# Kernel optimization log

Measured on AMD Instinct MI355X. Metric: run time of the kernel, lower is better.

Reference implementation:

```python
import jax, jax.numpy as jnp
import numpy as np

B, D_IN, D_OUT, N_SUBNET, G = 16384, 512, 512, 8, 2


def setup_inputs() -> dict:
    key = jax.random.key(0)
    k_x, k_g, k_w = jax.random.split(key, 3)
    x = jax.random.normal(k_x, (B, D_IN), dtype=jnp.float32)
    groups = jax.random.randint(k_g, (B, G), 0, N_SUBNET, dtype=jnp.int32)
    # per-expert Dense params (the 'subnets')
    W = jax.random.normal(k_w, (N_SUBNET, D_IN, D_OUT), dtype=jnp.float32) * (1.0 / np.sqrt(D_IN))
    b = jnp.zeros((N_SUBNET, D_OUT), dtype=jnp.float32)
    return {"x": x, "groups": groups, "W": W, "b": b}


def reference(x, groups, W, b):
    """SubnetGate: one-hot gated dispatch to per-group subnets + combine.

    Faithful math: gates = one_hot(groups[:, group_col], n_subnet);
    out = sum_e gates[:, e] * subnet_e(x). Since gates are one-hot the
    combine selects exactly one expert output per row (gate weight 1.0).
    """
    group_col = 0
    n_subnet = W.shape[0]
    idx_group = groups[:, group_col]                     # [B]
    gates = jax.nn.one_hot(idx_group, n_subnet, dtype=x.dtype)  # [B, E]
    # run every expert on the full batch (dense reference for the
    # gather-compute-scatter kernel), then gate-combine
    expert_out = jnp.einsum("bi,eio->beo", x, W) + b[None, :, :]  # [B, E, O]
    out = jnp.einsum("be,beo->bo", gates, expert_out)             # [B, O]
    return out
```

## Files before the change

### kernel.cpp

```cpp
#include <hip/hip_runtime.h>
#include <hip/hip_bf16.h>


#define NROWS   16384
#define KDIM    512
#define NDIM    512
#define NEXP    8
#define TILE_ELEMS 8192
#define ATILE_ELEMS 4096
#define MAX_DESC 264
#define WS_NDESC_OFF   64
#define WS_DESC_OFF    128
#define WS_ROWLIST_OFF 4096
#define WS_WT_OFF      (4096 + NEXP * NROWS * 4)
#define WS_XG_OFF      (WS_WT_OFF + NEXP * KDIM * NDIM * 2)
#define WS_NEED        ((size_t)WS_XG_OFF + (size_t)MAX_DESC * 8 * ATILE_ELEMS * 2)

typedef __bf16        bf16x8 __attribute__((ext_vector_type(8)));
typedef float         f32x4  __attribute__((ext_vector_type(4)));
typedef unsigned int  u32x4  __attribute__((ext_vector_type(4)));

__device__ __forceinline__ unsigned int f2bf_u(float f) {
    unsigned int u = __builtin_bit_cast(unsigned int, f);
    return (u + 0x7FFFu + ((u >> 16) & 1u)) >> 16;
}
__device__ __forceinline__ unsigned int pack2(float a, float b) {
    return f2bf_u(a) | (f2bf_u(b) << 16);
}
__device__ __forceinline__ u32x4 pack8(f32x4 a, f32x4 b) {
    u32x4 p;
    p.x = pack2(a.x, a.y); p.y = pack2(a.z, a.w);
    p.z = pack2(b.x, b.y); p.w = pack2(b.z, b.w);
    return p;
}
__device__ __forceinline__ void gl_lds16(const void* g, void* l) {
    __builtin_amdgcn_global_load_lds(
        (const __attribute__((address_space(1))) unsigned int*)g,
        (__attribute__((address_space(3))) unsigned int*)l, 16, 0, 0);
}

__global__ void zero_kernel(int* __restrict__ gcnt) {
    if (threadIdx.x < NEXP) gcnt[threadIdx.x] = 0;
}

__global__ void prep_kernel(const float* __restrict__ W,
                            const int* __restrict__ groups,
                            int* __restrict__ gcnt,
                            int* __restrict__ rowlist,
                            unsigned short* __restrict__ Wtile) {
    __shared__ __align__(16) unsigned short tl[TILE_ELEMS];
    __shared__ int lcnt[NEXP];
    __shared__ int lbase[NEXP];
    const int bid = blockIdx.x;
    const int tid = threadIdx.x;

    if (bid < 256) {
        const int e  = bid >> 5;
        const int nt = (bid >> 3) & 3;
        const int kt = bid & 7;
        const float* Wb = W + (size_t)e * (KDIM * NDIM);
        #pragma unroll
        for (int i = 0; i < 4; ++i) {
            int f = i * 256 + tid;
            int n = f & 127;
            int g = f >> 7;
            int col = nt * 128 + n;
            unsigned int p[4];
            #pragma unroll
            for (int jj = 0; jj < 4; ++jj) {
                int k0 = kt * 64 + g * 8 + jj * 2;
                p[jj] = pack2(Wb[(size_t)k0 * NDIM + col],
                              Wb[(size_t)(k0 + 1) * NDIM + col]);
            }
            *(u32x4*)&tl[n * 64 + (g ^ (n & 7)) * 8] = *(const u32x4*)p;
        }
        __syncthreads();
        unsigned short* dst = Wtile + (size_t)bid * TILE_ELEMS;
        #pragma unroll
        for (int i = 0; i < 4; ++i) {
            int off = (i * 256 + tid) * 8;
            *(u32x4*)&dst[off] = *(const u32x4*)&tl[off];
        }
    } else {
        const int base = (bid - 256) * 256;
        if (tid < NEXP) lcnt[tid] = 0;
        __syncthreads();
        int r = base + tid;
        int e = groups[r * 2];
        int pos = atomicAdd(&lcnt[e], 1);
        __syncthreads();
        if (tid < NEXP) lbase[tid] = atomicAdd(&gcnt[tid], lcnt[tid]);
        __syncthreads();
        rowlist[e * NROWS + lbase[e] + pos] = r;
    }
}

__global__ void plan_kernel(const int* __restrict__ counts,
                            int* __restrict__ ndesc,
                            int* __restrict__ desc) {
    if (threadIdx.x == 0) {
        int M = 0;
        for (int e = 0; e < NEXP; ++e) {
            int nmt = (counts[e] + 63) >> 6;
            for (int mt = 0; mt < nmt && M < MAX_DESC; ++mt)
                desc[M++] = (e << 16) | mt;
        }
        ndesc[0] = M;
    }
}

__global__ __launch_bounds__(256, 4)
void gather_kernel(const float* __restrict__ x,
                   const int* __restrict__ counts,
                   const int* __restrict__ rowlist,
                   const int* __restrict__ ndesc,
                   const int* __restrict__ desc,
                   unsigned short* __restrict__ xg) {
    const int bid = blockIdx.x;
    const int d  = bid >> 3;
    const int kt = bid & 7;
    if (d >= ndesc[0]) return;
    const int de = desc[d];
    const int e  = de >> 16;
    const int mt = de & 0xffff;
    const int cnt = counts[e];
    int m_valid = cnt - mt * 64;
    if (m_valid > 64) m_valid = 64;
    const int* rl = rowlist + e * NROWS + mt * 64;

    const int t = threadIdx.x;
    const int m = t >> 2;
    const int c = t & 3;

    u32x4 lo = {0u,0u,0u,0u}, hi = {0u,0u,0u,0u};
    if (m < m_valid) {
        const float* s = x + (size_t)rl[m] * KDIM + kt * 64 + c * 16;
        f32x4 v0 = *(const f32x4*)(s);
        f32x4 v1 = *(const f32x4*)(s + 4);
        f32x4 v2 = *(const f32x4*)(s + 8);
        f32x4 v3 = *(const f32x4*)(s + 12);
        lo = pack8(v0, v1);
        hi = pack8(v2, v3);
    }
    const int p = m & 7;
    unsigned short* tile = xg + ((size_t)d * 8 + kt) * ATILE_ELEMS;
    int base = (m * 8 + ((2 * c) ^ (p & 6))) * 8;
    if (p & 1) {
        *(u32x4*)&tile[base]     = hi;
        *(u32x4*)&tile[base + 8] = lo;
    } else {
        *(u32x4*)&tile[base]     = lo;
        *(u32x4*)&tile[base + 8] = hi;
    }
}

__global__ __launch_bounds__(256, 4)
void gemm_tiled(const unsigned short* __restrict__ xg,
                const int* __restrict__ counts,
                const int* __restrict__ rowlist,
                const unsigned short* __restrict__ Wtile,
                const float* __restrict__ bias,
                float* __restrict__ out,
                const int* __restrict__ ndesc,
                const int* __restrict__ desc) {
    __shared__ __align__(16) unsigned short Asm[ATILE_ELEMS];
    __shared__ __align__(16) unsigned short Bsm[TILE_ELEMS];

    const int tid = threadIdx.x;
    const int w   = tid >> 6;
    const int ln  = tid & 63;
    const int q   = ln >> 4;
    const int l15 = ln & 15;
    const int wm  = (w >> 1) * 32;
    const int wn  = (w & 1) * 64;

    const int T = ndesc[0] * 4;
    for (int tix = blockIdx.x; tix < T; tix += gridDim.x) {
        const int d  = tix >> 2;
        const int nt = tix & 3;
        const int de = desc[d];
        const int e  = de >> 16;
        const int mt = de & 0xffff;
        const int cnt = counts[e];
        int m_valid = cnt - mt * 64;
        if (m_valid > 64) m_valid = 64;
        const int* rl = rowlist + e * NROWS + mt * 64;

        const unsigned short* atile = xg + (size_t)d * 8 * ATILE_ELEMS;
        const unsigned short* btile = Wtile + (size_t)(e * 32 + nt * 8) * TILE_ELEMS;

        f32x4 acc[2][4];
        #pragma unroll
        for (int mi = 0; mi < 2; ++mi)
            #pragma unroll
            for (int ni = 0; ni < 4; ++ni)
                acc[mi][ni] = (f32x4){0.f, 0.f, 0.f, 0.f};

        #pragma unroll 1
        for (int kt = 0; kt < 8; ++kt) {
            const unsigned short* asrc = atile + kt * ATILE_ELEMS;
            const unsigned short* bsrc = btile + kt * TILE_ELEMS;
            #pragma unroll
            for (int i = 0; i < 2; ++i) {
                int off = (i * 256 + tid) * 8;
                gl_lds16(asrc + off, &Asm[off]);
            }
            #pragma unroll
            for (int i = 0; i < 4; ++i) {
                int off = (i * 256 + tid) * 8;
                gl_lds16(bsrc + off, &Bsm[off]);
            }
            __syncthreads();
            #pragma unroll
            for (int ks = 0; ks < 2; ++ks) {
                const int g = ks * 4 + q;
                bf16x8 af[2], bfr[4];
                #pragma unroll
                for (int mi = 0; mi < 2; ++mi) {
                    int r = wm + mi * 16 + l15;
                    af[mi] = *(const bf16x8*)&Asm[(r * 8 + (g ^ (r & 7))) * 8];
                }
                #pragma unroll
                for (int ni = 0; ni < 4; ++ni) {
                    int n = wn + ni * 16 + l15;
                    bfr[ni] = *(const bf16x8*)&Bsm[n * 64 + (g ^ (n & 7)) * 8];
                }
                #pragma unroll
                for (int mi = 0; mi < 2; ++mi)
                    #pragma unroll
                    for (int ni = 0; ni < 4; ++ni)
                        acc[mi][ni] = __builtin_amdgcn_mfma_f32_16x16x32_bf16(
                            af[mi], bfr[ni], acc[mi][ni], 0, 0, 0);
            }
            __syncthreads();
        }

        int growv[8];
        #pragma unroll
        for (int mi = 0; mi < 2; ++mi)
            #pragma unroll
            for (int r = 0; r < 4; ++r) {
                int rloc = wm + mi * 16 + q * 4 + r;
                growv[mi * 4 + r] = (rloc < m_valid) ? rl[rloc] : -1;
            }
        const int ncol0 = nt * 128 + wn;
        #pragma unroll
        for (int ni = 0; ni < 4; ++ni) {
            int col = ncol0 + ni * 16 + l15;
            float bv = bias[e * NDIM + col];
            #pragma unroll
            for (int mi = 0; mi < 2; ++mi)
                #pragma unroll
                for (int r = 0; r < 4; ++r) {
                    int gr = growv[mi * 4 + r];
                    if (gr >= 0) out[(size_t)gr * NDIM + col] = acc[mi][ni][r] + bv;
                }
        }
    }
}

__global__ __launch_bounds__(256, 2)
void gemm_fb(const float* __restrict__ x,
             const int* __restrict__ counts,
             const int* __restrict__ rowlist,
             const unsigned short* __restrict__ Wtile,
             const float* __restrict__ bias,
             float* __restrict__ out) {
    __shared__ __align__(16) unsigned short Asm[128 * 72];
    __shared__ __align__(16) unsigned short Bsm[TILE_ELEMS];

    const int bid = blockIdx.x;
    const int e   = bid >> 9;
    const int mt  = (bid >> 2) & 127;
    const int nt  = bid & 3;
    const int cnt = counts[e];
    const int rb  = mt * 128;
    if (rb >= cnt) return;
    int m_valid = cnt - rb;
    if (m_valid > 128) m_valid = 128;
    const int* rl = rowlist + e * NROWS + rb;

    const int tid = threadIdx.x;
    const int w   = tid >> 6;
    const int ln  = tid & 63;
    const int q   = ln >> 4;
    const int l15 = ln & 15;
    const int wm  = (w >> 1) * 64;
    const int wn  = (w & 1) * 64;

    const float* srcp[4];
    int lm[4], lg[4];
    #pragma unroll
    for (int i = 0; i < 4; ++i) {
        int f = i * 256 + tid;
        lm[i] = f >> 3;
        lg[i] = f & 7;
        srcp[i] = (lm[i] < m_valid) ? (x + (size_t)rl[lm[i]] * KDIM + lg[i] * 8)
                                    : nullptr;
    }
    const unsigned short* wt = Wtile + (size_t)(e * 32 + nt * 8) * TILE_ELEMS;

    f32x4 acc[4][4];
    #pragma unroll
    for (int mi = 0; mi < 4; ++mi)
        #pragma unroll
        for (int ni = 0; ni < 4; ++ni)
            acc[mi][ni] = (f32x4){0.f, 0.f, 0.f, 0.f};

    for (int kt = 0; kt < 8; ++kt) {
        const unsigned short* wsrc = wt + (size_t)kt * TILE_ELEMS;
        #pragma unroll
        for (int i = 0; i < 4; ++i) {
            int off = (i * 256 + tid) * 8;
            gl_lds16(wsrc + off, &Bsm[off]);
        }
        #pragma unroll
        for (int i = 0; i < 4; ++i) {
            u32x4 p = {0u, 0u, 0u, 0u};
            if (srcp[i]) {
                const float* s = srcp[i] + kt * 64;
                p = pack8(*(const f32x4*)s, *(const f32x4*)(s + 4));
            }
            *(u32x4*)&Asm[lm[i] * 72 + lg[i] * 8] = p;
        }
        __syncthreads();
        #pragma unroll
        for (int ks = 0; ks < 2; ++ks) {
            const int g = ks * 4 + q;
            bf16x8 af[4], bfr[4];
            #pragma unroll
            for (int mi = 0; mi < 4; ++mi)
                af[mi] = *(const bf16x8*)&Asm[(wm + mi * 16 + l15) * 72 + g * 8];
            #pragma unroll
            for (int ni = 0; ni < 4; ++ni) {
                int n = wn + ni * 16 + l15;
                bfr[ni] = *(const bf16x8*)&Bsm[n * 64 + (g ^ (n & 7)) * 8];
            }
            #pragma unroll
            for (int mi = 0; mi < 4; ++mi)
                #pragma unroll
                for (int ni = 0; ni < 4; ++ni)
                    acc[mi][ni] = __builtin_amdgcn_mfma_f32_16x16x32_bf16(
                        af[mi], bfr[ni], acc[mi][ni], 0, 0, 0);
        }
        __syncthreads();
    }

    int growv[16];
    #pragma unroll
    for (int mi = 0; mi < 4; ++mi)
        #pragma unroll
        for (int r = 0; r < 4; ++r) {
            int rloc = wm + mi * 16 + q * 4 + r;
            growv[mi * 4 + r] = (rloc < m_valid) ? rl[rloc] : -1;
        }
    const int ncol0 = nt * 128 + wn;
    #pragma unroll
    for (int ni = 0; ni < 4; ++ni) {
        int col = ncol0 + ni * 16 + l15;
        float bv = bias[e * NDIM + col];
        #pragma unroll
        for (int mi = 0; mi < 4; ++mi)
            #pragma unroll
            for (int r = 0; r < 4; ++r) {
                int gr = growv[mi * 4 + r];
                if (gr >= 0) out[(size_t)gr * NDIM + col] = acc[mi][ni][r] + bv;
            }
    }
}

extern "C" void kernel_launch(void* const* d_in, const int* in_sizes, int n_in,
                              void* d_out, int out_size, void* d_ws, size_t ws_size,
                              hipStream_t stream) {
    const float* x      = (const float*)d_in[0];
    const int*   groups = (const int*)d_in[1];
    const float* W      = (const float*)d_in[2];
    const float* b      = (const float*)d_in[3];
    float*       out    = (float*)d_out;

    char* ws = (char*)d_ws;
    int*            counts  = (int*)ws;
    int*            ndesc   = (int*)(ws + WS_NDESC_OFF);
    int*            desc    = (int*)(ws + WS_DESC_OFF);
    int*            rowlist = (int*)(ws + WS_ROWLIST_OFF);
    unsigned short* Wtile   = (unsigned short*)(ws + WS_WT_OFF);
    unsigned short* xg      = (unsigned short*)(ws + WS_XG_OFF);

    zero_kernel<<<1, 64, 0, stream>>>(counts);
    prep_kernel<<<320, 256, 0, stream>>>(W, groups, counts, rowlist, Wtile);
    plan_kernel<<<1, 64, 0, stream>>>(counts, ndesc, desc);
    if (ws_size >= WS_NEED) {
        gather_kernel<<<MAX_DESC * 8, 256, 0, stream>>>(x, counts, rowlist,
                                                        ndesc, desc, xg);
        gemm_tiled<<<MAX_DESC * 4, 256, 0, stream>>>(xg, counts, rowlist,
                                                     Wtile, b, out, ndesc, desc);
    } else {
        gemm_fb<<<4096, 256, 0, stream>>>(x, counts, rowlist, Wtile, b, out);
    }
}
```

Measured before the change: 131.1 us.

## Double-buffer LDS tiles to overlap next K-tile loads with MFMA compute

Splits the A and B shared-memory tiles into two buffers. The next K-tile's global-to-LDS copies are issued right after the current fragments are read into registers and before the MFMAs run, so load latency can hide behind compute. This removes one barrier per K step. In exchange it doubles LDS use per block and lowers the launch-bounds occupancy hint from 4 to 3 blocks per CU.

```diff
diff --git a/kernel.cpp b/kernel.cpp
--- a/kernel.cpp
+++ b/kernel.cpp
@@ -154,7 +154,7 @@
     }
 }
 
-__global__ __launch_bounds__(256, 4)
+__global__ __launch_bounds__(256, 3)
 void gemm_tiled(const unsigned short* __restrict__ xg,
                 const int* __restrict__ counts,
                 const int* __restrict__ rowlist,
@@ -163,8 +163,8 @@
                 float* __restrict__ out,
                 const int* __restrict__ ndesc,
                 const int* __restrict__ desc) {
-    __shared__ __align__(16) unsigned short Asm[ATILE_ELEMS];
-    __shared__ __align__(16) unsigned short Bsm[TILE_ELEMS];
+    __shared__ __align__(16) unsigned short Asm[2][ATILE_ELEMS];
+    __shared__ __align__(16) unsigned short Bsm[2][TILE_ELEMS];
 
     const int tid = threadIdx.x;
     const int w   = tid >> 6;
@@ -196,42 +196,59 @@
             for (int ni = 0; ni < 4; ++ni)
                 acc[mi][ni] = (f32x4){0.f, 0.f, 0.f, 0.f};
 
+        #pragma unroll
+        for (int i = 0; i < 2; ++i) {
+            int off = (i * 256 + tid) * 8;
+            gl_lds16(atile + off, &Asm[0][off]);
+        }
+        #pragma unroll
+        for (int i = 0; i < 4; ++i) {
+            int off = (i * 256 + tid) * 8;
+            gl_lds16(btile + off, &Bsm[0][off]);
+        }
+        __syncthreads();
+
         #pragma unroll 1
         for (int kt = 0; kt < 8; ++kt) {
-            const unsigned short* asrc = atile + kt * ATILE_ELEMS;
-            const unsigned short* bsrc = btile + kt * TILE_ELEMS;
-            #pragma unroll
-            for (int i = 0; i < 2; ++i) {
-                int off = (i * 256 + tid) * 8;
-                gl_lds16(asrc + off, &Asm[off]);
-            }
-            #pragma unroll
-            for (int i = 0; i < 4; ++i) {
-                int off = (i * 256 + tid) * 8;
-                gl_lds16(bsrc + off, &Bsm[off]);
-            }
-            __syncthreads();
+            const int cur = kt & 1;
+            bf16x8 af[2][2], bfr[2][4];
             #pragma unroll
             for (int ks = 0; ks < 2; ++ks) {
                 const int g = ks * 4 + q;
-                bf16x8 af[2], bfr[4];
                 #pragma unroll
                 for (int mi = 0; mi < 2; ++mi) {
                     int r = wm + mi * 16 + l15;
-                    af[mi] = *(const bf16x8*)&Asm[(r * 8 + (g ^ (r & 7))) * 8];
+                    af[ks][mi] = *(const bf16x8*)&Asm[cur][(r * 8 + (g ^ (r & 7))) * 8];
                 }
                 #pragma unroll
                 for (int ni = 0; ni < 4; ++ni) {
                     int n = wn + ni * 16 + l15;
-                    bfr[ni] = *(const bf16x8*)&Bsm[n * 64 + (g ^ (n & 7)) * 8];
+                    bfr[ks][ni] = *(const bf16x8*)&Bsm[cur][n * 64 + (g ^ (n & 7)) * 8];
                 }
+            }
+            __builtin_amdgcn_sched_barrier(0);
+            if (kt < 7) {
+                const unsigned short* an = atile + (kt + 1) * ATILE_ELEMS;
+                const unsigned short* bn = btile + (kt + 1) * TILE_ELEMS;
+                #pragma unroll
+                for (int i = 0; i < 2; ++i) {
+                    int off = (i * 256 + tid) * 8;
+                    gl_lds16(an + off, &Asm[cur ^ 1][off]);
+                }
+                #pragma unroll
+                for (int i = 0; i < 4; ++i) {
+                    int off = (i * 256 + tid) * 8;
+                    gl_lds16(bn + off, &Bsm[cur ^ 1][off]);
+                }
+            }
+            #pragma unroll
+            for (int ks = 0; ks < 2; ++ks)
                 #pragma unroll
                 for (int mi = 0; mi < 2; ++mi)
                     #pragma unroll
                     for (int ni = 0; ni < 4; ++ni)
                         acc[mi][ni] = __builtin_amdgcn_mfma_f32_16x16x32_bf16(
-                            af[mi], bfr[ni], acc[mi][ni], 0, 0, 0);
-            }
+                            af[ks][mi], bfr[ks][ni], acc[mi][ni], 0, 0, 0);
             __syncthreads();
         }
 
```

New measurement: 130.2 us. Within noise of the previous version (-0.6%).
